# Optimization experiments

Measured on AMD Instinct MI355X. Metric: run time of the kernel, lower is better.

## Reference

```python
import jax, jax.numpy as jnp
from jax import lax
import numpy as np

B, C_IN, H, W = 32, 128, 64, 64
C_OUT, K, KH, KW = 256, 4, 3, 3
HIDDEN = C_IN  # in_planes != 3 -> hidden_planes = in_planes
T_TEMP = 34.0
BN_EPS = 1e-5


def setup_inputs() -> dict:
    key = jax.random.key(0)
    ks = jax.random.split(key, 4)
    return {
        "x": jax.random.normal(ks[0], (B, C_IN, H, W), dtype=jnp.float32),
        "w_fc1": jax.random.normal(ks[1], (HIDDEN, C_IN), dtype=jnp.float32) * (2.0 / C_IN) ** 0.5,
        "bn1_gamma": jnp.ones((HIDDEN,), jnp.float32),
        "bn1_beta": jnp.zeros((HIDDEN,), jnp.float32),
        "bn1_mean": jnp.zeros((HIDDEN,), jnp.float32),
        "bn1_var": jnp.ones((HIDDEN,), jnp.float32),
        "w_fc2": jax.random.normal(ks[2], (K * C_IN, HIDDEN), dtype=jnp.float32) * (2.0 / HIDDEN) ** 0.5,
        "b_fc2": jnp.zeros((K * C_IN,), jnp.float32),
        "bn2_gamma": jnp.ones((K * C_IN,), jnp.float32),
        "bn2_beta": jnp.zeros((K * C_IN,), jnp.float32),
        "bn2_mean": jnp.zeros((K * C_IN,), jnp.float32),
        "bn2_var": jnp.ones((K * C_IN,), jnp.float32),
        "anchored_w": jax.random.normal(ks[3], (K, C_OUT, C_IN, KH, KW), dtype=jnp.float32) * (2.0 / (C_OUT * KH * KW)) ** 0.5,
        "anchored_b": jnp.zeros((K, C_OUT), jnp.float32),
    }


def _bn(v, gamma, beta, mean, var):
    return (v - mean) * gamma * lax.rsqrt(var + BN_EPS) + beta


def reference(x, w_fc1, bn1_gamma, bn1_beta, bn1_mean, bn1_var,
              w_fc2, b_fc2, bn2_gamma, bn2_beta, bn2_mean, bn2_var,
              anchored_w, anchored_b):
    # ----- CFG routing: squeeze-excite style softmax over K*C_in -----
    pooled = x.mean(axis=(2, 3))                      # [B, C_in]  (adaptive avg pool to 1x1)
    h = pooled @ w_fc1.T                              # [B, hidden] (1x1 conv, no bias)
    h = jax.nn.relu(_bn(h, bn1_gamma, bn1_beta, bn1_mean, bn1_var))
    t = h @ w_fc2.T + b_fc2                           # [B, K*C_in]
    t = _bn(t, bn2_gamma, bn2_beta, bn2_mean, bn2_var)
    theta = jax.nn.softmax(t / T_TEMP, axis=1)        # [B, K*C_in]
    theta_r = theta.reshape(-1, K, anchored_w.shape[2])  # [B, K, C_in]

    # ----- per-sample kernel mixture: sum_k theta[b,k,i] * W[k,o,i,h,w] -----
    w = jnp.einsum('bki,koihw->boihw', theta_r, anchored_w)  # [B, C_out, C_in, KH, KW]
    b = theta_r.mean(axis=2) @ anchored_b                    # [B, C_out]

    # ----- per-sample conv (equiv. to grouped conv with groups=B) -----
    def conv1(xi, wi):
        return lax.conv_general_dilated(
            xi[None], wi, window_strides=(1, 1), padding=((1, 1), (1, 1)),
            dimension_numbers=('NCHW', 'OIHW', 'NCHW'))[0]

    out = jax.vmap(conv1)(x, w) + b[:, :, None, None]  # [B, C_out, H, W]
    return out
```

## Files before the change

### kernel.cpp

```cpp
#include <hip/hip_runtime.h>
#include <hip/hip_bf16.h>

typedef __attribute__((ext_vector_type(8))) __bf16 bf16x8;
typedef __attribute__((ext_vector_type(4))) float f32x4;

__device__ __forceinline__ unsigned pk2bf(float lo, float hi) {
  __hip_bfloat162 h = __float22bfloat162_rn(make_float2(lo, hi));
  unsigned u;
  __builtin_memcpy(&u, &h, 4);
  return u;
}

__device__ __forceinline__ void gload_lds16(const void* g, void* l) {
  __builtin_amdgcn_global_load_lds(
      (const __attribute__((address_space(1))) unsigned int*)g,
      (__attribute__((address_space(3))) unsigned int*)l, 16, 0, 0);
}

__global__ __launch_bounds__(256) void k_pool_convert(
    const float* __restrict__ x, float* __restrict__ psum,
    unsigned short* __restrict__ xbf) {
  __shared__ float xs[128][65];
  const int b = blockIdx.x >> 6;
  const int y = blockIdx.x & 63;
  const int t = threadIdx.x;
  const float* src = x + ((size_t)b * 128) * 4096 + y * 64;
#pragma unroll
  for (int i = 0; i < 8; ++i) {
    int idx = t + i * 256;
    int c = idx >> 4, x4 = (idx & 15) << 2;
    float4 v = *(const float4*)(src + (size_t)c * 4096 + x4);
    xs[c][x4] = v.x; xs[c][x4 + 1] = v.y; xs[c][x4 + 2] = v.z; xs[c][x4 + 3] = v.w;
  }
  __syncthreads();
  if (t < 128) {
    float s = 0.f;
#pragma unroll
    for (int j = 0; j < 64; ++j) s += xs[t][j];
    psum[((size_t)b * 128 + t) * 64 + y] = s;
  }
#pragma unroll
  for (int i = 0; i < 4; ++i) {
    int idx = t + i * 256;
    int q = idx & 3, xx = (idx >> 2) & 63, g = idx >> 8;
    unsigned wd[4];
#pragma unroll
    for (int j = 0; j < 4; ++j)
      wd[j] = pk2bf(xs[g * 32 + q * 8 + 2 * j][xx], xs[g * 32 + q * 8 + 2 * j + 1][xx]);
    *(uint4*)(xbf + ((((size_t)b * 4 + g) * 4096) + y * 64 + xx) * 32 + q * 8) =
        make_uint4(wd[0], wd[1], wd[2], wd[3]);
  }
}

__global__ __launch_bounds__(128) void k_route(
    const float* __restrict__ psum, const float* __restrict__ w_fc1,
    const float* __restrict__ g1, const float* __restrict__ be1,
    const float* __restrict__ m1, const float* __restrict__ v1,
    const float* __restrict__ w_fc2, const float* __restrict__ bfc2,
    const float* __restrict__ g2, const float* __restrict__ be2,
    const float* __restrict__ m2, const float* __restrict__ v2,
    const float* __restrict__ ab, float* __restrict__ theta,
    float* __restrict__ bias) {
  __shared__ float pooled[128], hs[128], r2[8];
  const int b = blockIdx.x, t = threadIdx.x;
  const int wid = t >> 6;
  float s = 0.f;
  const float* ps = psum + ((size_t)b * 128 + t) * 64;
  for (int j = 0; j < 64; ++j) s += ps[j];
  pooled[t] = s * (1.0f / 4096.0f);
  __syncthreads();
  float acc = 0.f;
  const float* w1r = w_fc1 + t * 128;
  for (int i = 0; i < 128; ++i) acc += pooled[i] * w1r[i];
  acc = (acc - m1[t]) * g1[t] * rsqrtf(v1[t] + 1e-5f) + be1[t];
  hs[t] = fmaxf(acc, 0.f);
  __syncthreads();
  float tv[4];
  for (int q = 0; q < 4; ++q) {
    int m = q * 128 + t;
    const float* w2r = w_fc2 + (size_t)m * 128;
    float a2 = bfc2[m];
    for (int i = 0; i < 128; ++i) a2 += hs[i] * w2r[i];
    a2 = (a2 - m2[m]) * g2[m] * rsqrtf(v2[m] + 1e-5f) + be2[m];
    tv[q] = a2 * (1.0f / 34.0f);
  }
  float mx4 = fmaxf(fmaxf(tv[0], tv[1]), fmaxf(tv[2], tv[3]));
  for (int o = 32; o; o >>= 1) mx4 = fmaxf(mx4, __shfl_xor(mx4, o));
  if ((t & 63) == 0) r2[wid] = mx4;
  __syncthreads();
  float mx = fmaxf(r2[0], r2[1]);
  float e[4], ss = 0.f;
  for (int q = 0; q < 4; ++q) { e[q] = expf(tv[q] - mx); ss += e[q]; }
  for (int o = 32; o; o >>= 1) ss += __shfl_xor(ss, o);
  if ((t & 63) == 0) r2[2 + wid] = ss;
  __syncthreads();
  float inv = 1.0f / (r2[2] + r2[3]);
  float th[4], tk[4];
  for (int q = 0; q < 4; ++q) { th[q] = e[q] * inv; theta[b * 512 + q * 128 + t] = th[q]; }
  for (int q = 0; q < 4; ++q) {
    float v = th[q];
    for (int o = 32; o; o >>= 1) v += __shfl_xor(v, o);
    tk[q] = v;
  }
  __syncthreads();
  if ((t & 63) == 0)
    for (int q = 0; q < 4; ++q) r2[wid * 4 + q] = tk[q];
  __syncthreads();
  for (int o = t; o < 256; o += 128) {
    float bb = 0.f;
    for (int k = 0; k < 4; ++k) bb += (r2[k] + r2[4 + k]) * (1.0f / 128.0f) * ab[k * 256 + o];
    bias[b * 256 + o] = bb;
  }
}

__global__ __launch_bounds__(256) void k_mix(
    const float* __restrict__ aw, const float* __restrict__ theta,
    unsigned short* __restrict__ wmix) {
  __shared__ float aw_s[4][32][33];
  __shared__ float th_s[32][4][32];
  const int bx = blockIdx.x;
  const int oq = bx & 3, obl = (bx >> 2) & 1, ks = bx >> 3;
  const int g = ks / 9, tt = ks % 9;
  const int tid = threadIdx.x;
#pragma unroll
  for (int i = 0; i < 16; ++i) {
    int e = tid + i * 256;
    int i32 = e & 31, o32 = (e >> 5) & 31, k = e >> 10;
    aw_s[k][i32][o32] =
        aw[((size_t)((k * 256 + obl * 128 + oq * 32 + o32) * 128) + g * 32 + i32) * 9 + tt];
    int kb = (e >> 5) & 3, bb = e >> 7;
    th_s[bb][kb][i32] = theta[bb * 512 + kb * 128 + g * 32 + i32];
  }
  __syncthreads();
  for (int it = 0; it < 16; ++it) {
    int b = it * 2 + (tid >> 7);
    int u = tid & 127;
    int o32 = u >> 2, q = u & 3;
    unsigned wd[4];
#pragma unroll
    for (int jj = 0; jj < 4; ++jj) {
      int i0 = q * 8 + jj * 2, i1 = i0 + 1;
      float v0 = th_s[b][0][i0] * aw_s[0][i0][o32] + th_s[b][1][i0] * aw_s[1][i0][o32]
               + th_s[b][2][i0] * aw_s[2][i0][o32] + th_s[b][3][i0] * aw_s[3][i0][o32];
      float v1 = th_s[b][0][i1] * aw_s[0][i1][o32] + th_s[b][1][i1] * aw_s[1][i1][o32]
               + th_s[b][2][i1] * aw_s[2][i1][o32] + th_s[b][3][i1] * aw_s[3][i1][o32];
      wd[jj] = pk2bf(v0, v1);
    }
    unsigned A = (unsigned)(((oq * 32 + o32) * 32 + q * 8) * 2);
    unsigned P = A ^ ((A >> 2) & 0x70u);
    size_t tilebase = (((size_t)b * 36 + ks) * 2 + obl) * 8192;
    *(uint4*)((char*)wmix + tilebase + P) = make_uint4(wd[0], wd[1], wd[2], wd[3]);
  }
}

__global__ __launch_bounds__(256, 2) void k_conv(
    const unsigned short* __restrict__ xbf, const unsigned short* __restrict__ wmix,
    const float* __restrict__ bias, float* __restrict__ out) {
  __shared__ __align__(16) char xls[21120];
  __shared__ __align__(16) char wls[2][16384];
  const int bx = blockIdx.x;
  const int wgid = ((bx & 7) << 7) | (bx >> 3);
  const int b = wgid >> 5, pblk = wgid & 31;
  const int tid = threadIdx.x;
  const int lane = tid & 63, wv = tid >> 6;
  const int y0 = pblk << 1;
  const int l15 = lane & 15, l4 = lane >> 4;

  unsigned a_off0 = ((unsigned)(l15 * 64 + l4 * 16)) ^ ((unsigned)(l15 & 7) << 4);
  a_off0 += (unsigned)(wv * 4096);

  f32x4 acc[4][8] = {};

  const unsigned short* xsrc_b = xbf + (size_t)b * 4 * 4096 * 32;

  auto stageW = [&](int ks, int buf) {
    const char* wsrc = (const char*)wmix + (size_t)(b * 36 + ks) * 16384;
#pragma unroll
    for (int p = 0; p < 4; ++p)
      gload_lds16(wsrc + p * 4096 + wv * 1024 + lane * 16,
                  wls[buf] + p * 4096 + wv * 1024);
  };

  uint4 xr[5];
  auto loadX = [&](int g) {
    const unsigned short* xsrc = xsrc_b + (size_t)g * (4096 * 32);
#pragma unroll
    for (int i = 0; i < 4; ++i) {
      int e = tid + i * 256;
      int q = e & 3, rc = e >> 2, c = rc % 66, r = rc / 66;
      int yy = y0 - 1 + r, xx = c - 1;
      uint4 v = make_uint4(0u, 0u, 0u, 0u);
      if ((unsigned)yy < 64u && (unsigned)xx < 64u)
        v = *(const uint4*)(xsrc + (((size_t)yy << 6) + xx) * 32 + q * 8);
      xr[i] = v;
    }
    if (tid < 32) {
      int e = tid + 1024;
      int q = e & 3, rc = e >> 2, c = rc % 66, r = rc / 66;
      int yy = y0 - 1 + r, xx = c - 1;
      uint4 v = make_uint4(0u, 0u, 0u, 0u);
      if ((unsigned)yy < 64u && (unsigned)xx < 64u)
        v = *(const uint4*)(xsrc + (((size_t)yy << 6) + xx) * 32 + q * 8);
      xr[4] = v;
    }
  };
  auto writeX = [&]() {
#pragma unroll
    for (int i = 0; i < 4; ++i) {
      int e = tid + i * 256;
      int q = e & 3, rc = e >> 2, c = rc % 66, r = rc / 66;
      *(uint4*)(xls + (r * 66 + c) * 80 + q * 16) = xr[i];
    }
    if (tid < 32) {
      int e = tid + 1024;
      int q = e & 3, rc = e >> 2, c = rc % 66, r = rc / 66;
      *(uint4*)(xls + (r * 66 + c) * 80 + q * 16) = xr[4];
    }
  };

  loadX(0);
  writeX();
  stageW(0, 0);
  asm volatile("s_waitcnt lgkmcnt(0)" ::: "memory");

#pragma unroll
  for (int ks = 0; ks < 36; ++ks) {
    asm volatile("s_waitcnt vmcnt(0)" ::: "memory");
    __builtin_amdgcn_s_barrier();
    asm volatile("" ::: "memory");
    if (ks > 0 && ks % 9 == 0) {
      writeX();
      asm volatile("s_waitcnt lgkmcnt(0)" ::: "memory");
      __builtin_amdgcn_s_barrier();
      asm volatile("" ::: "memory");
    }
    if (ks % 9 == 8 && ks < 35) {
      loadX(ks / 9 + 1);
      asm volatile("" ::: "memory");
    }
    if (ks + 1 < 36) stageW(ks + 1, (ks + 1) & 1);
    const int dy = (ks % 9) / 3, dx = (ks % 9) % 3;
    bf16x8 bfr[8], afr[4];
    const char* bbase = xls + ((0 + dy) * 66 + dx + l15) * 80 + l4 * 16;
#pragma unroll
    for (int pf = 0; pf < 4; ++pf) bfr[pf] = *(const bf16x8*)(bbase + pf * 1280);
#pragma unroll
    for (int pf = 0; pf < 4; ++pf) bfr[pf + 4] = *(const bf16x8*)(bbase + 5280 + pf * 1280);
    const char* abase = wls[ks & 1] + a_off0;
#pragma unroll
    for (int of = 0; of < 4; ++of) afr[of] = *(const bf16x8*)(abase + of * 1024);
    __builtin_amdgcn_s_setprio(1);
#pragma unroll
    for (int of = 0; of < 4; ++of)
#pragma unroll
      for (int pf = 0; pf < 8; ++pf)
        acc[of][pf] = __builtin_amdgcn_mfma_f32_16x16x32_bf16(afr[of], bfr[pf], acc[of][pf], 0, 0, 0);
    __builtin_amdgcn_s_setprio(0);
  }

  const float* bp = bias + b * 256 + wv * 64;
  float bv[4][4];
#pragma unroll
  for (int of = 0; of < 4; ++of)
#pragma unroll
    for (int j = 0; j < 4; ++j) bv[of][j] = bp[of * 16 + l4 * 4 + j];
  size_t outbase = ((size_t)(b * 256 + wv * 64)) * 4096 + (size_t)y0 * 64;
#pragma unroll
  for (int of = 0; of < 4; ++of)
#pragma unroll
    for (int pf = 0; pf < 8; ++pf) {
      int py = pf >> 2, px0 = (pf & 3) * 16;
#pragma unroll
      for (int j = 0; j < 4; ++j)
        out[outbase + (size_t)(of * 16 + l4 * 4 + j) * 4096 + py * 64 + px0 + l15] =
            acc[of][pf][j] + bv[of][j];
    }
}

extern "C" void kernel_launch(void* const* d_in, const int* in_sizes, int n_in,
                              void* d_out, int out_size, void* d_ws, size_t ws_size,
                              hipStream_t stream) {
  const float* x     = (const float*)d_in[0];
  const float* w_fc1 = (const float*)d_in[1];
  const float* g1    = (const float*)d_in[2];
  const float* be1   = (const float*)d_in[3];
  const float* m1    = (const float*)d_in[4];
  const float* v1    = (const float*)d_in[5];
  const float* w_fc2 = (const float*)d_in[6];
  const float* bfc2  = (const float*)d_in[7];
  const float* g2    = (const float*)d_in[8];
  const float* be2   = (const float*)d_in[9];
  const float* m2    = (const float*)d_in[10];
  const float* v2    = (const float*)d_in[11];
  const float* aw    = (const float*)d_in[12];
  const float* ab    = (const float*)d_in[13];
  float* out = (float*)d_out;

  char* ws = (char*)d_ws;
  unsigned short* xbf  = (unsigned short*)(ws);
  unsigned short* wmix = (unsigned short*)(ws + 33554432);
  float* psum  = (float*)(ws + 52428800);
  float* theta = (float*)(ws + 53477376);
  float* bias  = (float*)(ws + 53542912);

  hipLaunchKernelGGL(k_pool_convert, dim3(2048), dim3(256), 0, stream, x, psum, xbf);
  hipLaunchKernelGGL(k_route, dim3(32), dim3(128), 0, stream, psum, w_fc1, g1, be1, m1, v1,
                     w_fc2, bfc2, g2, be2, m2, v2, ab, theta, bias);
  hipLaunchKernelGGL(k_mix, dim3(288), dim3(256), 0, stream, aw, theta, wmix);
  hipLaunchKernelGGL(k_conv, dim3(1024), dim3(256), 0, stream, xbf, wmix, bias, out);
}
```

Before: 130.6 us.

## Replace double-buffered weight staging with single LDS buffer and synchronous load

Removes the second LDS buffer for mixed weights and restructures the k-step loop so each step stages its own weight tile, waits for it, and then computes. This cuts LDS usage and may raise occupancy, but it gives up the overlap between loading the next weight tile and the MFMA work. It also adds a second barrier to every step.

```diff
diff --git a/kernel.cpp b/kernel.cpp
--- a/kernel.cpp
+++ b/kernel.cpp
@@ -157,7 +157,7 @@
     const unsigned short* __restrict__ xbf, const unsigned short* __restrict__ wmix,
     const float* __restrict__ bias, float* __restrict__ out) {
   __shared__ __align__(16) char xls[21120];
-  __shared__ __align__(16) char wls[2][16384];
+  __shared__ __align__(16) char wls[16384];
   const int bx = blockIdx.x;
   const int wgid = ((bx & 7) << 7) | (bx >> 3);
   const int b = wgid >> 5, pblk = wgid & 31;
@@ -173,12 +173,12 @@
 
   const unsigned short* xsrc_b = xbf + (size_t)b * 4 * 4096 * 32;
 
-  auto stageW = [&](int ks, int buf) {
+  auto stageW = [&](int ks) {
     const char* wsrc = (const char*)wmix + (size_t)(b * 36 + ks) * 16384;
 #pragma unroll
     for (int p = 0; p < 4; ++p)
       gload_lds16(wsrc + p * 4096 + wv * 1024 + lane * 16,
-                  wls[buf] + p * 4096 + wv * 1024);
+                  wls + p * 4096 + wv * 1024);
   };
 
   uint4 xr[5];
@@ -220,33 +220,39 @@
 
   loadX(0);
   writeX();
-  stageW(0, 0);
-  asm volatile("s_waitcnt lgkmcnt(0)" ::: "memory");
+  stageW(0);
+  asm volatile("s_waitcnt vmcnt(0) lgkmcnt(0)" ::: "memory");
+  __builtin_amdgcn_s_barrier();
+  asm volatile("" ::: "memory");
 
 #pragma unroll
   for (int ks = 0; ks < 36; ++ks) {
-    asm volatile("s_waitcnt vmcnt(0)" ::: "memory");
-    __builtin_amdgcn_s_barrier();
-    asm volatile("" ::: "memory");
-    if (ks > 0 && ks % 9 == 0) {
-      writeX();
-      asm volatile("s_waitcnt lgkmcnt(0)" ::: "memory");
+    const int g = ks / 9, t = ks % 9;
+    if (ks > 0) {
       __builtin_amdgcn_s_barrier();
       asm volatile("" ::: "memory");
-    }
-    if (ks % 9 == 8 && ks < 35) {
-      loadX(ks / 9 + 1);
+      stageW(ks);
+      if (t == 0) {
+        writeX();
+        asm volatile("s_waitcnt vmcnt(0) lgkmcnt(0)" ::: "memory");
+      } else {
+        asm volatile("s_waitcnt vmcnt(0)" ::: "memory");
+      }
+      __builtin_amdgcn_s_barrier();
       asm volatile("" ::: "memory");
     }
-    if (ks + 1 < 36) stageW(ks + 1, (ks + 1) & 1);
-    const int dy = (ks % 9) / 3, dx = (ks % 9) % 3;
+    if (t == 8 && g < 3) {
+      loadX(g + 1);
+      asm volatile("" ::: "memory");
+    }
+    const int dy = t / 3, dx = t % 3;
     bf16x8 bfr[8], afr[4];
-    const char* bbase = xls + ((0 + dy) * 66 + dx + l15) * 80 + l4 * 16;
+    const char* bbase = xls + (dy * 66 + dx + l15) * 80 + l4 * 16;
 #pragma unroll
     for (int pf = 0; pf < 4; ++pf) bfr[pf] = *(const bf16x8*)(bbase + pf * 1280);
 #pragma unroll
     for (int pf = 0; pf < 4; ++pf) bfr[pf + 4] = *(const bf16x8*)(bbase + 5280 + pf * 1280);
-    const char* abase = wls[ks & 1] + a_off0;
+    const char* abase = wls + a_off0;
 #pragma unroll
     for (int of = 0; of < 4; ++of) afr[of] = *(const bf16x8*)(abase + of * 1024);
     __builtin_amdgcn_s_setprio(1);
```

Result: slower. 151.3 us (+15.9%).
